# Optimization experiments

Measured on AMD Instinct MI355X. Metric: run time of the kernel, lower is better.

## Reference

```python
import jax, jax.numpy as jnp
import numpy as np

DIM = 1024
DIM_LATENT = 1024
DIM_HEAD = 64
INNER = max(DIM, DIM_LATENT)  # 1024
HEADS = INNER // DIM_HEAD     # 16
SCALE = DIM_HEAD ** -0.5
LN_EPS = 1e-5
RMS_EPS = 1e-8


def layernorm(x, g, b):
    mu = jnp.mean(x, axis=-1, keepdims=True)
    var = jnp.mean(jnp.square(x - mu), axis=-1, keepdims=True)
    return (x - mu) * jax.lax.rsqrt(var + LN_EPS) * g + b


def rmsnorm(x, gamma):
    # torch: x / clamp(norm(x,-1) * d**-0.5, eps) * gamma
    n = jnp.linalg.norm(x, axis=-1, keepdims=True) * (x.shape[-1] ** -0.5)
    return x / jnp.maximum(n, RMS_EPS) * gamma


def setup_inputs() -> dict:
    key = jax.random.key(0)
    ks = jax.random.split(key, 8)
    b, n, nl = 8, 2048, 512
    x = jax.random.normal(ks[0], (b, n, DIM), dtype=jnp.float32)
    latents = jax.random.normal(ks[1], (b, nl, DIM_LATENT), dtype=jnp.float32)
    mask = jax.random.randint(ks[2], (b, n), 0, 2).astype(bool)
    init = lambda k, shape, fan_in: jax.random.normal(k, shape, jnp.float32) * (fan_in ** -0.5)
    return {
        "x": x,
        "latents": latents,
        "mask": mask,
        "ln_x_g": jnp.ones((DIM,), jnp.float32),
        "ln_x_b": jnp.zeros((DIM,), jnp.float32),
        "ln_l_g": jnp.ones((DIM_LATENT,), jnp.float32),
        "ln_l_b": jnp.zeros((DIM_LATENT,), jnp.float32),
        "q_gamma": jnp.ones((DIM_HEAD,), jnp.float32),
        "k_gamma": jnp.ones((DIM_HEAD,), jnp.float32),
        "W_q": init(ks[3], (DIM_LATENT, INNER), DIM_LATENT),
        "W_kv": init(ks[4], (DIM, 2 * INNER), DIM),
        "W_out": init(ks[5], (INNER, DIM_LATENT), INNER),
        "b_out": jnp.zeros((DIM_LATENT,), jnp.float32),
    }


def reference(x, latents, mask, ln_x_g, ln_x_b, ln_l_g, ln_l_b,
              q_gamma, k_gamma, W_q, W_kv, W_out, b_out):
    b, n, _ = x.shape
    nl = latents.shape[1]
    xn = layernorm(x, ln_x_g, ln_x_b)
    ln = layernorm(latents, ln_l_g, ln_l_b)

    q = ln @ W_q                                   # [b, nl, inner]
    kv = jnp.concatenate([xn @ W_kv, ln @ W_kv], axis=1)  # [b, n+nl, 2*inner]
    k, v = kv[..., :INNER], kv[..., INNER:]

    to_heads = lambda t: t.reshape(t.shape[0], t.shape[1], HEADS, DIM_HEAD).transpose(0, 2, 1, 3)
    q, k, v = to_heads(q), to_heads(k), to_heads(v)  # [b, h, *, d]

    qn = rmsnorm(q, q_gamma) * SCALE
    kn = rmsnorm(k, k_gamma)

    sim = jnp.einsum('bhid,bhjd->bhij', qn, kn)      # [b, h, nl, n+nl]
    full_mask = jnp.pad(mask, ((0, 0), (0, nl)), constant_values=True)
    neg = -jnp.finfo(sim.dtype).max
    sim = jnp.where(full_mask[:, None, None, :], sim, neg)

    attn = jax.nn.softmax(sim.astype(jnp.float32), axis=-1).astype(sim.dtype)
    out = jnp.einsum('bhij,bhjd->bhid', attn, v)     # [b, h, nl, d]
    out = out.transpose(0, 2, 1, 3).reshape(b, nl, INNER)
    return out @ W_out + b_out
```

## Files before the change

### kernel.cpp

```cpp
#include <hip/hip_runtime.h>
#include <hip/hip_bf16.h>
#include <cfloat>
#include <cmath>

typedef __hip_bfloat16 bf16;
#define DEV_INLINE __device__ __forceinline__

typedef __attribute__((ext_vector_type(8))) short short8;
typedef __attribute__((ext_vector_type(4))) short short4v;
typedef __attribute__((ext_vector_type(4))) float float4v;
typedef __attribute__((ext_vector_type(16))) float float16v;

#define BATCH 8
#define NSEQ 2048
#define NLAT 512
#define DIM_ 1024
#define NKV 2560
#define HEADS_ 16
#define DHEAD 64
#define SCALE_ 0.125f
#define LN_EPS_ 1e-5f
#define RMS_EPS_ 1e-8f

DEV_INLINE float bf2f(bf16 v) { return __bfloat162float(v); }
DEV_INLINE bf16 f2bf(float v) { return __float2bfloat16(v); }
DEV_INLINE short bfbits(float x) { union { bf16 b; short s; } c; c.b = f2bf(x); return c.s; }
DEV_INLINE float sbits2f(short s) { union { bf16 b; short s; } c; c.s = s; return bf2f(c.b); }

DEV_INLINE int detect_bf16(const void* ones) {
    return (*(const unsigned*)ones == 0x3F803F80u) ? 1 : 0;
}

template<typename T> DEV_INLINE float ldf(const T* p);
template<> DEV_INLINE float ldf<float>(const float* p) { return *p; }
template<> DEV_INLINE float ldf<bf16>(const bf16* p)  { return __bfloat162float(*p); }

DEV_INLINE void gload16(const bf16* g, bf16* l) {
    __builtin_amdgcn_global_load_lds(
        (const __attribute__((address_space(1))) unsigned int*)g,
        (__attribute__((address_space(3))) unsigned int*)l,
        16, 0, 0);
}

DEV_INLINE float block_sum_256(float v, float* sred) {
    #pragma unroll
    for (int o = 1; o < 64; o <<= 1) v += __shfl_xor(v, o, 64);
    int w = threadIdx.x >> 6;
    __syncthreads();
    if ((threadIdx.x & 63) == 0) sred[w] = v;
    __syncthreads();
    return sred[0] + sred[1] + sred[2] + sred[3];
}

template<typename T>
DEV_INLINE void ln_row_body(int r, const void* xv, const void* latv,
                            const void* gxv, const void* bxv,
                            const void* glv, const void* blv,
                            bf16* __restrict__ out, float* sred)
{
    const T* src; const T* g; const T* be; bf16* o;
    if (r < BATCH * NSEQ) {
        int b = r >> 11, i = r & 2047;
        src = (const T*)xv + (size_t)r * DIM_;
        o = out + ((size_t)b * NKV + i) * DIM_;
        g = (const T*)gxv; be = (const T*)bxv;
    } else {
        int rr = r - BATCH * NSEQ;
        int b = rr >> 9, i = rr & 511;
        src = (const T*)latv + (size_t)rr * DIM_;
        o = out + ((size_t)b * NKV + NSEQ + i) * DIM_;
        g = (const T*)glv; be = (const T*)blv;
    }
    int t = threadIdx.x;
    float v[4];
    float s = 0.f;
    #pragma unroll
    for (int j = 0; j < 4; j++) { v[j] = ldf(src + t + j * 256); s += v[j]; }
    s = block_sum_256(s, sred);
    float mu = s * (1.f / 1024.f);
    float s2 = 0.f;
    #pragma unroll
    for (int j = 0; j < 4; j++) { float d = v[j] - mu; s2 += d * d; }
    s2 = block_sum_256(s2, sred);
    float rstd = rsqrtf(s2 * (1.f / 1024.f) + LN_EPS_);
    #pragma unroll
    for (int j = 0; j < 4; j++) {
        int c = t + j * 256;
        o[c] = f2bf((v[j] - mu) * rstd * ldf(g + c) + ldf(be + c));
    }
}

template<typename T>
DEV_INLINE void trans_body(int bid, const void* wqv, const void* wkvv, const void* woutv,
                           bf16* wqT, bf16* wkvT, bf16* woutT, float* tile )
{
    const T* in; bf16* out; int N, t0;
    if (bid < 1024)      { in = (const T*)wqv;   out = wqT;   N = 1024; t0 = bid; }
    else if (bid < 3072) { in = (const T*)wkvv;  out = wkvT;  N = 2048; t0 = bid - 1024; }
    else                 { in = (const T*)woutv; out = woutT; N = 1024; t0 = bid - 3072; }
    int K = 1024;
    int nb = N >> 5;
    int bn = (t0 % nb) * 32, bk = (t0 / nb) * 32;
    int tx = threadIdx.x & 31, ty = threadIdx.x >> 5;
    #pragma unroll
    for (int j = 0; j < 4; j++)
        tile[(ty + j * 8) * 33 + tx] = ldf(in + (size_t)(bk + ty + j * 8) * N + bn + tx);
    __syncthreads();
    #pragma unroll
    for (int j = 0; j < 4; j++)
        out[(size_t)(bn + ty + j * 8) * K + bk + tx] = f2bf(tile[tx * 33 + ty + j * 8]);
}

__global__ __launch_bounds__(256) void prep_kernel(
    const void* x, const void* lat,
    const void* gx, const void* bx, const void* gl, const void* bl,
    const void* wq, const void* wkv, const void* wout,
    bf16* __restrict__ cat_n, bf16* __restrict__ wqT,
    bf16* __restrict__ wkvT, bf16* __restrict__ woutT)
{
    __shared__ float smem[32 * 33];
    int isb = detect_bf16(gx);
    int bid = blockIdx.x;
    if (bid < 20480) {
        if (isb) ln_row_body<bf16>(bid, x, lat, gx, bx, gl, bl, cat_n, smem);
        else     ln_row_body<float>(bid, x, lat, gx, bx, gl, bl, cat_n, smem);
    } else {
        int t = bid - 20480;
        if (isb) trans_body<bf16>(t, wq, wkv, wout, wqT, wkvT, woutT, smem);
        else     trans_body<float>(t, wq, wkv, wout, wqT, wkvT, woutT, smem);
    }
}

#define MFMA_CORE_128(As, Bs, Apt, Bpt, K, acc)                                \
    {                                                                          \
        bf16* Asl_ = &As[threadIdx.x * 8];                                     \
        bf16* Bsl_ = &Bs[threadIdx.x * 8];                                     \
        for (int k0 = 0; k0 < K; k0 += 64) {                                   \
            __syncthreads();                                                   \
            _Pragma("unroll")                                                  \
            for (int rep = 0; rep < 4; rep++) {                                \
                gload16(Apt[rep] + k0, Asl_ + rep * 2048);                     \
                gload16(Bpt[rep] + k0, Bsl_ + rep * 2048);                     \
            }                                                                  \
            __syncthreads();                                                   \
            _Pragma("unroll")                                                  \
            for (int kk = 0; kk < 4; kk++) {                                   \
                short8 af_[2], bf_[2];                                         \
                _Pragma("unroll")                                              \
                for (int ms = 0; ms < 2; ms++) {                               \
                    int row = wm * 64 + ms * 32 + l32;                         \
                    int jc = (kk * 2 + h5) ^ (row & 7);                        \
                    af_[ms] = *(const short8*)&As[row * 64 + jc * 8];          \
                }                                                              \
                _Pragma("unroll")                                              \
                for (int ns = 0; ns < 2; ns++) {                               \
                    int row = wn * 64 + ns * 32 + l32;                         \
                    int jc = (kk * 2 + h5) ^ (row & 7);                        \
                    bf_[ns] = *(const short8*)&Bs[row * 64 + jc * 8];          \
                }                                                              \
                _Pragma("unroll")                                              \
                for (int ms = 0; ms < 2; ms++)                                 \
                    _Pragma("unroll")                                          \
                    for (int ns = 0; ns < 2; ns++)                             \
                        acc[ms][ns] = __builtin_amdgcn_mfma_f32_32x32x16_bf16( \
                            af_[ms], bf_[ns], acc[ms][ns], 0, 0, 0);           \
            }                                                                  \
        }                                                                      \
    }

__global__ __launch_bounds__(256) void gemm_qkv(
    const void* gq, const void* gk,
    const bf16* __restrict__ cat_n, const bf16* __restrict__ wkvT,
    const bf16* __restrict__ wqT,
    bf16* __restrict__ kbuf, bf16* __restrict__ vtbuf, bf16* __restrict__ qbuf)
{
    __shared__ bf16 As[128 * 64];
    __shared__ bf16 Bs[128 * 64];
    int isb = detect_bf16(gq);

    int tid = threadIdx.x;
    int bid = blockIdx.x;
    int wv = tid >> 6, lane = tid & 63, l32 = lane & 31, h5 = lane >> 5;
    int wm = wv >> 1, wn = wv & 1;

    const bf16* Bt; int bn, bm; bool isq;
    if (bid < 2560) { bn = bid & 15; bm = bid >> 4; Bt = wkvT; isq = false; }
    else { int t = bid - 2560; bn = t & 7; bm = t >> 3; Bt = wqT; isq = true; }
    const int K = 1024;

    const bf16* Apt[4]; const bf16* Bpt[4];
    #pragma unroll
    for (int rep = 0; rep < 4; rep++) {
        int c = rep * 256 + tid;
        int row = c >> 3;
        int k8 = ((c & 7) ^ (row & 7)) * 8;
        int ar = bm * 128 + row;
        int am = isq ? ((ar >> 9) * NKV + NSEQ + (ar & 511)) : ar;
        Apt[rep] = cat_n + (size_t)am * K + k8;
        Bpt[rep] = Bt + (size_t)(bn * 128 + row) * K + k8;
    }

    float16v acc[2][2];
    #pragma unroll
    for (int i = 0; i < 2; i++)
        #pragma unroll
        for (int j = 0; j < 2; j++)
            #pragma unroll
            for (int r = 0; r < 16; r++) acc[i][j][r] = 0.f;

    MFMA_CORE_128(As, Bs, Apt, Bpt, K, acc);

    bool dorms = isq || (bn < 8);
    if (dorms) {
        const void* gp = isq ? gq : gk;
        float g2[2];
        #pragma unroll
        for (int ns = 0; ns < 2; ns++) {
            int idx = ns * 32 + l32;
            g2[ns] = isb ? bf2f(((const bf16*)gp)[idx]) : ((const float*)gp)[idx];
        }
        #pragma unroll
        for (int ms = 0; ms < 2; ms++) {
            #pragma unroll
            for (int reg = 0; reg < 16; reg++) {
                float ss = acc[ms][0][reg] * acc[ms][0][reg]
                         + acc[ms][1][reg] * acc[ms][1][reg];
                ss += __shfl_xor(ss, 1, 64);
                ss += __shfl_xor(ss, 2, 64);
                ss += __shfl_xor(ss, 4, 64);
                ss += __shfl_xor(ss, 8, 64);
                ss += __shfl_xor(ss, 16, 64);
                float n = sqrtf(ss) * 0.125f;
                float inv = 1.0f / fmaxf(n, RMS_EPS_);
                if (isq) inv *= SCALE_;
                acc[ms][0][reg] *= inv * g2[0];
                acc[ms][1][reg] *= inv * g2[1];
            }
        }
    }

    if (!isq && bn >= 8) {
        int bq = bm / 20;
        int keyb = (bm % 20) * 128 + wm * 64;
        #pragma unroll
        for (int ms = 0; ms < 2; ms++) {
            #pragma unroll
            for (int rg = 0; rg < 4; rg++) {
                int key = keyb + ms * 32 + rg * 8 + h5 * 4;
                #pragma unroll
                for (int ns = 0; ns < 2; ns++) {
                    int col = bn * 128 + wn * 64 + ns * 32 + l32 - 1024;
                    int h = col >> 6, d = col & 63;
                    short4v ov;
                    #pragma unroll
                    for (int rr = 0; rr < 4; rr++) ov[rr] = bfbits(acc[ms][ns][rg * 4 + rr]);
                    *(short4v*)(vtbuf + ((size_t)((bq * 16 + h) * 64 + d)) * NKV + key) = ov;
                }
            }
        }
    } else {
        bf16* C = isq ? qbuf : kbuf;
        #pragma unroll
        for (int ms = 0; ms < 2; ms++) {
            #pragma unroll
            for (int rg = 0; rg < 4; rg++) {
                int row0 = bm * 128 + wm * 64 + ms * 32 + rg * 8 + h5 * 4;
                #pragma unroll
                for (int rr = 0; rr < 4; rr++) {
                    int row = row0 + rr;
                    #pragma unroll
                    for (int ns = 0; ns < 2; ns++) {
                        int col = bn * 128 + wn * 64 + ns * 32 + l32;
                        C[(size_t)row * 1024 + col] = f2bf(acc[ms][ns][rg * 4 + rr]);
                    }
                }
            }
        }
    }
}

#define KC 64
__global__ __launch_bounds__(256) void attn_mfma(
    const bf16* __restrict__ q, const bf16* __restrict__ kbuf,
    const bf16* __restrict__ vtbuf, const int* __restrict__ maskp,
    const void* gk, bf16* __restrict__ out)
{
    __shared__ bf16 Ks[KC * 64];
    __shared__ bf16 Vt[DHEAD * 64];
    __shared__ bf16 Ps[4][2][16][64];
    __shared__ float msk_s[KC];

    int isb = detect_bf16(gk);
    int tid = threadIdx.x;
    int bid = blockIdx.x;
    int bh = bid & 127, qb = bid >> 7;
    int h = bh & 15, bb = bh >> 4;
    int wv = tid >> 6, lane = tid & 63, quad = lane >> 4, l16 = lane & 15;
    int q8 = quad * 8;
    int qbase = qb * 128 + wv * 32;
    int sw = l16 & 7;

    const bf16* kbase = kbuf + (size_t)bb * NKV * 1024 + h * DHEAD;
    const bf16* vbase = vtbuf + (size_t)(bb * 16 + h) * DHEAD * NKV;

    short8 qf[2][2];
    #pragma unroll
    for (int qt = 0; qt < 2; qt++) {
        const bf16* qp = q + ((size_t)(bb * NLAT + qbase + qt * 16 + l16)) * 1024 + h * DHEAD;
        qf[qt][0] = *(const short8*)(qp + q8);
        qf[qt][1] = *(const short8*)(qp + q8 + 32);
    }

    float gv = isb ? bf2f(((const bf16*)gk)[lane]) : ((const float*)gk)[lane];
    gv = fabsf(gv);
    #pragma unroll
    for (int o = 1; o < 64; o <<= 1) gv = fmaxf(gv, __shfl_xor(gv, o, 64));
    float m_fix[2];
    #pragma unroll
    for (int qt = 0; qt < 2; qt++) {
        float ssq = 0.f;
        #pragma unroll
        for (int j = 0; j < 8; j++) {
            float a = sbits2f(qf[qt][0][j]);
            float b = sbits2f(qf[qt][1][j]);
            ssq += a * a + b * b;
        }
        ssq += __shfl_xor(ssq, 16, 64);
        ssq += __shfl_xor(ssq, 32, 64);
        m_fix[qt] = sqrtf(ssq) * 8.0f * gv;
    }

    int c0 = tid, c1 = tid + 256;
    int krow0 = c0 >> 3, kj0 = ((c0 & 7) ^ (krow0 & 7)) * 8;
    int krow1 = c1 >> 3, kj1 = ((c1 & 7) ^ (krow1 & 7)) * 8;

    float4v o_acc[2][4];
    #pragma unroll
    for (int qt = 0; qt < 2; qt++)
        #pragma unroll
        for (int ds = 0; ds < 4; ds++)
            #pragma unroll
            for (int r = 0; r < 4; r++) o_acc[qt][ds][r] = 0.f;
    float l_i[2] = {0.f, 0.f};

    for (int kb = 0; kb < NKV; kb += KC) {
        __syncthreads();
        gload16(kbase + (size_t)(kb + krow0) * 1024 + kj0, &Ks[c0 * 8]);
        gload16(kbase + (size_t)(kb + krow1) * 1024 + kj1, &Ks[c1 * 8]);
        gload16(vbase + (size_t)krow0 * NKV + kb + kj0, &Vt[c0 * 8]);
        gload16(vbase + (size_t)krow1 * NKV + kb + kj1, &Vt[c1 * 8]);
        if (tid < KC) {
            int key = kb + tid;
            float mv = 0.f;
            if (key < NSEQ) mv = maskp[bb * NSEQ + key] ? 0.f : -1e30f;
            msk_s[tid] = mv;
        }
        __syncthreads();

        float4v st[2][4];
        #pragma unroll
        for (int kt = 0; kt < 4; kt++) {
            int row = kt * 16 + l16;
            short8 kf0 = *(const short8*)&Ks[row * 64 + ((quad ^ sw) << 3)];
            short8 kf1 = *(const short8*)&Ks[row * 64 + (((quad + 4) ^ sw) << 3)];
            #pragma unroll
            for (int qt = 0; qt < 2; qt++) {
                float4v z; z[0]=0.f; z[1]=0.f; z[2]=0.f; z[3]=0.f;
                z = __builtin_amdgcn_mfma_f32_16x16x32_bf16(kf0, qf[qt][0], z, 0, 0, 0);
                z = __builtin_amdgcn_mfma_f32_16x16x32_bf16(kf1, qf[qt][1], z, 0, 0, 0);
                st[qt][kt] = z;
            }
        }
        float4 mv4[4];
        #pragma unroll
        for (int kt = 0; kt < 4; kt++) mv4[kt] = *(const float4*)&msk_s[kt * 16 + 4 * quad];
        #pragma unroll
        for (int qt = 0; qt < 2; qt++) {
            float lp = 0.f;
            #pragma unroll
            for (int kt = 0; kt < 4; kt++) {
                const float* mk = (const float*)&mv4[kt];
                short4v pk;
                #pragma unroll
                for (int r = 0; r < 4; r++) {
                    float e = __expf(st[qt][kt][r] + mk[r] - m_fix[qt]);
                    lp += e;
                    pk[r] = bfbits(e);
                }
                int j = kt * 2 + (quad >> 1);
                int js = j ^ sw;
                *(short4v*)&Ps[wv][qt][l16][js * 8 + (quad & 1) * 4] = pk;
            }
            l_i[qt] += lp;
        }

        #pragma unroll
        for (int kc = 0; kc < 2; kc++) {
            short8 pf[2];
            #pragma unroll
            for (int qt = 0; qt < 2; qt++)
                pf[qt] = *(const short8*)&Ps[wv][qt][l16][((kc * 4 + quad) ^ sw) * 8];
            #pragma unroll
            for (int ds = 0; ds < 4; ds++) {
                int row = ds * 16 + l16;
                short8 vf = *(const short8*)&Vt[row * 64 + (((kc * 4 + quad) ^ sw) << 3)];
                #pragma unroll
                for (int qt = 0; qt < 2; qt++)
                    o_acc[qt][ds] = __builtin_amdgcn_mfma_f32_16x16x32_bf16(vf, pf[qt], o_acc[qt][ds], 0, 0, 0);
            }
        }
    }

    #pragma unroll
    for (int qt = 0; qt < 2; qt++) {
        float l = l_i[qt];
        l += __shfl_xor(l, 16, 64);
        l += __shfl_xor(l, 32, 64);
        float inv = 1.0f / l;
        bf16* op = out + ((size_t)(bb * NLAT + qbase + qt * 16 + l16)) * 1024 + h * DHEAD;
        #pragma unroll
        for (int ds = 0; ds < 4; ds++) {
            short4v ov;
            #pragma unroll
            for (int r = 0; r < 4; r++) ov[r] = bfbits(o_acc[qt][ds][r] * inv);
            *(short4v*)(op + ds * 16 + 4 * quad) = ov;
        }
    }
}

__global__ __launch_bounds__(256) void gemm_out(
    const void* ones, const void* bias,
    const bf16* __restrict__ A, const bf16* __restrict__ Bt, void* __restrict__ Cout)
{
    __shared__ bf16 As[128 * 64];
    __shared__ bf16 Bs[128 * 64];
    int isb = detect_bf16(ones);

    int tid = threadIdx.x;
    int bn = blockIdx.x, bm = blockIdx.y;
    int wv = tid >> 6, lane = tid & 63, l32 = lane & 31, h5 = lane >> 5;
    int wm = wv >> 1, wn = wv & 1;
    const int K = 1024, N = 1024;

    const bf16* Apt[4]; const bf16* Bpt[4];
    #pragma unroll
    for (int rep = 0; rep < 4; rep++) {
        int c = rep * 256 + tid;
        int row = c >> 3;
        int k8 = ((c & 7) ^ (row & 7)) * 8;
        Apt[rep] = A + (size_t)(bm * 128 + row) * K + k8;
        Bpt[rep] = Bt + (size_t)(bn * 128 + row) * K + k8;
    }

    float16v acc[2][2];
    #pragma unroll
    for (int i = 0; i < 2; i++)
        #pragma unroll
        for (int j = 0; j < 2; j++)
            #pragma unroll
            for (int r = 0; r < 16; r++) acc[i][j][r] = 0.f;

    MFMA_CORE_128(As, Bs, Apt, Bpt, K, acc);

    #pragma unroll
    for (int ms = 0; ms < 2; ms++) {
        #pragma unroll
        for (int rg = 0; rg < 4; rg++) {
            int row0 = bm * 128 + wm * 64 + ms * 32 + rg * 8 + h5 * 4;
            #pragma unroll
            for (int rr = 0; rr < 4; rr++) {
                int row = row0 + rr;
                #pragma unroll
                for (int ns = 0; ns < 2; ns++) {
                    int col = bn * 128 + wn * 64 + ns * 32 + l32;
                    float bv = isb ? bf2f(((const bf16*)bias)[col]) : ((const float*)bias)[col];
                    float v = acc[ms][ns][rg * 4 + rr] + bv;
                    if (isb) ((bf16*)Cout)[(size_t)row * N + col] = f2bf(v);
                    else     ((float*)Cout)[(size_t)row * N + col] = v;
                }
            }
        }
    }
}

extern "C" void kernel_launch(void* const* d_in, const int* in_sizes, int n_in,
                              void* d_out, int out_size, void* d_ws, size_t ws_size,
                              hipStream_t stream) {
    const int* mask = (const int*)d_in[2];

    char* ws = (char*)d_ws;
    size_t off = 0;
    bf16* cat_n   = (bf16*)(ws + off); off += (size_t)20480 * 1024 * 2;
    bf16* kbuf    = (bf16*)(ws + off); off += (size_t)20480 * 1024 * 2;
    bf16* vtbuf   = (bf16*)(ws + off); off += (size_t)8192 * 2560 * 2;
    bf16* qbuf    = (bf16*)(ws + off); off += (size_t)4096 * 1024 * 2;
    bf16* attnout = (bf16*)(ws + off); off += (size_t)4096 * 1024 * 2;
    bf16* wqT     = (bf16*)(ws + off); off += (size_t)1024 * 1024 * 2;
    bf16* wkvT    = (bf16*)(ws + off); off += (size_t)2048 * 1024 * 2;
    bf16* woutT   = (bf16*)(ws + off); off += (size_t)1024 * 1024 * 2;

    prep_kernel<<<24576, 256, 0, stream>>>(
        d_in[0], d_in[1], d_in[3], d_in[4], d_in[5], d_in[6],
        d_in[9], d_in[10], d_in[11], cat_n, wqT, wkvT, woutT);

    gemm_qkv<<<2816, 256, 0, stream>>>(
        d_in[7], d_in[8], cat_n, wkvT, wqT, kbuf, vtbuf, qbuf);

    attn_mfma<<<512, 256, 0, stream>>>(qbuf, kbuf, vtbuf, mask, d_in[8], attnout);

    gemm_out<<<dim3(8, 32), 256, 0, stream>>>(
        d_in[3], d_in[12], attnout, woutT, d_out);
}
```

Measured before the change: 373.7 us.

## Split attention KV range across two wave groups per block and merge partials

The attention kernel now launches 512 threads per block. Two groups of four waves each process half of the 2560 keys, each with its own K/V shared-memory tile. Because the softmax uses a fixed max, the partial outputs and sums are combined through shared memory at the end. Mask values are now read straight from global memory as int4 instead of being staged in shared memory. This doubles the number of waves per block to give more latency hiding on the 512-block grid, at the cost of a final reduction step and more shared memory per block.

```diff
diff --git a/kernel.cpp b/kernel.cpp
--- a/kernel.cpp
+++ b/kernel.cpp
@@ -280,15 +280,14 @@
 }
 
 #define KC 64
-__global__ __launch_bounds__(256) void attn_mfma(
+__global__ __launch_bounds__(512) void attn_mfma(
     const bf16* __restrict__ q, const bf16* __restrict__ kbuf,
     const bf16* __restrict__ vtbuf, const int* __restrict__ maskp,
     const void* gk, bf16* __restrict__ out)
 {
-    __shared__ bf16 Ks[KC * 64];
-    __shared__ bf16 Vt[DHEAD * 64];
-    __shared__ bf16 Ps[4][2][16][64];
-    __shared__ float msk_s[KC];
+    __shared__ bf16 Ks[2][KC * 64];
+    __shared__ bf16 Vt[2][DHEAD * 64];
+    __shared__ bf16 Ps[8][2][16][64];
 
     int isb = detect_bf16(gk);
     int tid = threadIdx.x;
@@ -296,8 +295,10 @@
     int bh = bid & 127, qb = bid >> 7;
     int h = bh & 15, bb = bh >> 4;
     int wv = tid >> 6, lane = tid & 63, quad = lane >> 4, l16 = lane & 15;
+    int kh = wv >> 2, wv2 = wv & 3;
+    int t2 = tid & 255;
     int q8 = quad * 8;
-    int qbase = qb * 128 + wv * 32;
+    int qbase = qb * 128 + wv2 * 32;
     int sw = l16 & 7;
 
     const bf16* kbase = kbuf + (size_t)bb * NKV * 1024 + h * DHEAD;
@@ -330,7 +331,7 @@
         m_fix[qt] = sqrtf(ssq) * 8.0f * gv;
     }
 
-    int c0 = tid, c1 = tid + 256;
+    int c0 = t2, c1 = t2 + 256;
     int krow0 = c0 >> 3, kj0 = ((c0 & 7) ^ (krow0 & 7)) * 8;
     int krow1 = c1 >> 3, kj1 = ((c1 & 7) ^ (krow1 & 7)) * 8;
 
@@ -343,26 +344,37 @@
             for (int r = 0; r < 4; r++) o_acc[qt][ds][r] = 0.f;
     float l_i[2] = {0.f, 0.f};
 
-    for (int kb = 0; kb < NKV; kb += KC) {
+    int kb0 = kh * 1280;
+    for (int it = 0; it < 20; it++) {
+        int kb = kb0 + it * KC;
         __syncthreads();
-        gload16(kbase + (size_t)(kb + krow0) * 1024 + kj0, &Ks[c0 * 8]);
-        gload16(kbase + (size_t)(kb + krow1) * 1024 + kj1, &Ks[c1 * 8]);
-        gload16(vbase + (size_t)krow0 * NKV + kb + kj0, &Vt[c0 * 8]);
-        gload16(vbase + (size_t)krow1 * NKV + kb + kj1, &Vt[c1 * 8]);
-        if (tid < KC) {
-            int key = kb + tid;
-            float mv = 0.f;
-            if (key < NSEQ) mv = maskp[bb * NSEQ + key] ? 0.f : -1e30f;
-            msk_s[tid] = mv;
-        }
+        gload16(kbase + (size_t)(kb + krow0) * 1024 + kj0, &Ks[kh][c0 * 8]);
+        gload16(kbase + (size_t)(kb + krow1) * 1024 + kj1, &Ks[kh][c1 * 8]);
+        gload16(vbase + (size_t)krow0 * NKV + kb + kj0, &Vt[kh][c0 * 8]);
+        gload16(vbase + (size_t)krow1 * NKV + kb + kj1, &Vt[kh][c1 * 8]);
         __syncthreads();
+
+        float4 mv4[4];
+        if (kb < NSEQ) {
+            #pragma unroll
+            for (int kt = 0; kt < 4; kt++) {
+                int4 mi = *(const int4*)(maskp + bb * NSEQ + kb + kt * 16 + quad * 4);
+                mv4[kt].x = mi.x ? 0.f : -1e30f;
+                mv4[kt].y = mi.y ? 0.f : -1e30f;
+                mv4[kt].z = mi.z ? 0.f : -1e30f;
+                mv4[kt].w = mi.w ? 0.f : -1e30f;
+            }
+        } else {
+            #pragma unroll
+            for (int kt = 0; kt < 4; kt++) { mv4[kt].x = 0.f; mv4[kt].y = 0.f; mv4[kt].z = 0.f; mv4[kt].w = 0.f; }
+        }
 
         float4v st[2][4];
         #pragma unroll
         for (int kt = 0; kt < 4; kt++) {
             int row = kt * 16 + l16;
-            short8 kf0 = *(const short8*)&Ks[row * 64 + ((quad ^ sw) << 3)];
-            short8 kf1 = *(const short8*)&Ks[row * 64 + (((quad + 4) ^ sw) << 3)];
+            short8 kf0 = *(const short8*)&Ks[kh][row * 64 + ((quad ^ sw) << 3)];
+            short8 kf1 = *(const short8*)&Ks[kh][row * 64 + (((quad + 4) ^ sw) << 3)];
             #pragma unroll
             for (int qt = 0; qt < 2; qt++) {
                 float4v z; z[0]=0.f; z[1]=0.f; z[2]=0.f; z[3]=0.f;
@@ -371,9 +383,6 @@
                 st[qt][kt] = z;
             }
         }
-        float4 mv4[4];
-        #pragma unroll
-        for (int kt = 0; kt < 4; kt++) mv4[kt] = *(const float4*)&msk_s[kt * 16 + 4 * quad];
         #pragma unroll
         for (int qt = 0; qt < 2; qt++) {
             float lp = 0.f;
@@ -403,7 +412,7 @@
             #pragma unroll
             for (int ds = 0; ds < 4; ds++) {
                 int row = ds * 16 + l16;
-                short8 vf = *(const short8*)&Vt[row * 64 + (((kc * 4 + quad) ^ sw) << 3)];
+                short8 vf = *(const short8*)&Vt[kh][row * 64 + (((kc * 4 + quad) ^ sw) << 3)];
                 #pragma unroll
                 for (int qt = 0; qt < 2; qt++)
                     o_acc[qt][ds] = __builtin_amdgcn_mfma_f32_16x16x32_bf16(vf, pf[qt], o_acc[qt][ds], 0, 0, 0);
@@ -411,19 +420,40 @@
         }
     }
 
-    #pragma unroll
-    for (int qt = 0; qt < 2; qt++) {
-        float l = l_i[qt];
-        l += __shfl_xor(l, 16, 64);
-        l += __shfl_xor(l, 32, 64);
-        float inv = 1.0f / l;
-        bf16* op = out + ((size_t)(bb * NLAT + qbase + qt * 16 + l16)) * 1024 + h * DHEAD;
-        #pragma unroll
-        for (int ds = 0; ds < 4; ds++) {
-            short4v ov;
-            #pragma unroll
-            for (int r = 0; r < 4; r++) ov[r] = bfbits(o_acc[qt][ds][r] * inv);
-            *(short4v*)(op + ds * 16 + 4 * quad) = ov;
+    __syncthreads();
+    float* fbuf = (float*)&Ps[0][0][0][0];
+    float* lbuf = (float*)&Ks[0][0];
+    int slot = wv2 * 64 + lane;
+    if (kh == 1) {
+        #pragma unroll
+        for (int qt = 0; qt < 2; qt++) {
+            #pragma unroll
+            for (int ds = 0; ds < 4; ds++)
+                #pragma unroll
+                for (int r = 0; r < 4; r++)
+                    fbuf[((qt * 4 + ds) * 4 + r) * 256 + slot] = o_acc[qt][ds][r];
+            lbuf[qt * 256 + slot] = l_i[qt];
+        }
+    }
+    __syncthreads();
+    if (kh == 0) {
+        #pragma unroll
+        for (int qt = 0; qt < 2; qt++) {
+            float l = l_i[qt] + lbuf[qt * 256 + slot];
+            l += __shfl_xor(l, 16, 64);
+            l += __shfl_xor(l, 32, 64);
+            float inv = 1.0f / l;
+            bf16* op = out + ((size_t)(bb * NLAT + qbase + qt * 16 + l16)) * 1024 + h * DHEAD;
+            #pragma unroll
+            for (int ds = 0; ds < 4; ds++) {
+                short4v ov;
+                #pragma unroll
+                for (int r = 0; r < 4; r++) {
+                    float v = o_acc[qt][ds][r] + fbuf[((qt * 4 + ds) * 4 + r) * 256 + slot];
+                    ov[r] = bfbits(v * inv);
+                }
+                *(short4v*)(op + ds * 16 + 4 * quad) = ov;
+            }
         }
     }
 }
@@ -506,7 +536,7 @@
     gemm_qkv<<<2816, 256, 0, stream>>>(
         d_in[7], d_in[8], cat_n, wkvT, wqT, kbuf, vtbuf, qbuf);
 
-    attn_mfma<<<512, 256, 0, stream>>>(qbuf, kbuf, vtbuf, mask, d_in[8], attnout);
+    attn_mfma<<<512, 512, 0, stream>>>(qbuf, kbuf, vtbuf, mask, d_in[8], attnout);
 
     gemm_out<<<dim3(8, 32), 256, 0, stream>>>(
         d_in[3], d_in[12], attnout, woutT, d_out);
```

New measurement: 413.8 us. 1.11x slower.
